# Kernel tuning notes

Hardware: AMD Instinct MI355X
Metric: run time of the kernel (lower is better)

Reference implementation:

```python
import jax, jax.numpy as jnp
import numpy as np

B, N, C = 4, 2047, 1024
H = 16
D = C // H  # head_dim = 64
SCALE = D ** -0.5


def setup_inputs() -> dict:
    key = jax.random.key(0)
    ks = jax.random.split(key, 5)
    return {
        "x": jax.random.normal(ks[0], (B, N, C), dtype=jnp.float32),
        "qkv_w": jax.random.normal(ks[1], (3 * C, C), dtype=jnp.float32) * (C ** -0.5),
        "proj_w": jax.random.normal(ks[2], (C, C), dtype=jnp.float32) * (C ** -0.5),
        "proj_b": jax.random.normal(ks[3], (C,), dtype=jnp.float32) * 0.02,
        "bias": jax.random.normal(ks[4], (H, N, N), dtype=jnp.float32) * 0.02,
    }


def reference(x, qkv_w, proj_w, proj_b, bias):
    b, n, c = x.shape
    qkv = (x @ qkv_w.T).reshape(b, n, 3, H, D)
    qkv = jnp.transpose(qkv, (2, 0, 3, 1, 4))
    q, k, v = qkv[0], qkv[1], qkv[2]
    q = q * SCALE
    # scores (B,H,N,N) + additive relative-position bias (H,N,N)
    attn = jnp.einsum('bhnd,bhmd->bhnm', q, k) + bias[None]
    attn = jax.nn.softmax(attn, axis=-1)
    out = jnp.einsum('bhnm,bhmd->bhnd', attn, v)
    out = jnp.transpose(out, (0, 2, 1, 3)).reshape(b, n, c)
    return out @ proj_w.T + proj_b
```

## Files before the change

### kernel.cpp

```cpp
#include <hip/hip_runtime.h>
#include <hip/hip_bf16.h>

typedef __bf16 bf16;
typedef __attribute__((ext_vector_type(8))) __bf16 bf16x8;
typedef __attribute__((ext_vector_type(4))) __bf16 bf16x4;
typedef __attribute__((ext_vector_type(4))) float f32x4;

#define MFMA16(a, b, c) __builtin_amdgcn_mfma_f32_16x16x32_bf16((a), (b), (c), 0, 0, 0)

constexpr int Bb = 4, Nn = 2047, Cc = 1024, Hh = 16, Dd = 64;
constexpr int M_ROWS = Bb * Nn;
constexpr int NPAD = 2048;
constexpr float SCALE = 0.125f;
constexpr float NEG_BIG = -1e30f;
constexpr float DEFER_THR = 8.0f;

template <bool V> struct BC { static constexpr bool value = V; };

__device__ inline bf16x8 bzero8() {
    bf16x8 v;
    for (int i = 0; i < 8; ++i) v[i] = (bf16)0.0f;
    return v;
}
__device__ inline bf16x8 bones8() {
    bf16x8 v;
    for (int i = 0; i < 8; ++i) v[i] = (bf16)1.0f;
    return v;
}
__device__ inline f32x4 fzero4() {
    f32x4 v = {0.f, 0.f, 0.f, 0.f};
    return v;
}

__device__ __forceinline__ void async_copy16(const void* g, void* l) {
    __builtin_amdgcn_global_load_lds(
        (const __attribute__((address_space(1))) unsigned int*)g,
        (__attribute__((address_space(3))) unsigned int*)l, 16, 0, 0);
}

__global__ __launch_bounds__(256) void cvt3_kernel(
    const float* __restrict__ a, bf16* __restrict__ oa, int na8,
    const float* __restrict__ b, bf16* __restrict__ ob, int nb8,
    const float* __restrict__ c, bf16* __restrict__ oc, int nc8) {
    int i = blockIdx.x * blockDim.x + threadIdx.x;
    const float* src;
    bf16* dst;
    int j = i;
    if (j < na8) {
        src = a; dst = oa;
    } else {
        j -= na8;
        if (j < nb8) {
            src = b; dst = ob;
        } else {
            j -= nb8;
            if (j >= nc8) return;
            src = c; dst = oc;
        }
    }
    float4 x0 = ((const float4*)src)[2 * (size_t)j];
    float4 x1 = ((const float4*)src)[2 * (size_t)j + 1];
    bf16x8 v;
    v[0] = (bf16)x0.x; v[1] = (bf16)x0.y; v[2] = (bf16)x0.z; v[3] = (bf16)x0.w;
    v[4] = (bf16)x1.x; v[5] = (bf16)x1.y; v[6] = (bf16)x1.z; v[7] = (bf16)x1.w;
    *(bf16x8*)(dst + 8 * (size_t)j) = v;
}

__global__ __launch_bounds__(256) void transpose_v_kernel(
    const bf16* __restrict__ vd, bf16* __restrict__ vtd) {
    __shared__ bf16 t[64 * 72];
    const int bh = blockIdx.x, nt = blockIdx.y;
    const int tid = threadIdx.x;
    const bf16* src = vd + (size_t)bh * Nn * Dd;
    bf16* dst = vtd + (size_t)bh * Dd * NPAD;
    int c = tid;
    for (int it = 0; it < 2; ++it, c += 256) {
        int row = c >> 3, d8 = (c & 7) * 8;
        int gn = nt * 64 + row;
        bf16x8 v = bzero8();
        if (gn < Nn) v = *(const bf16x8*)(src + (size_t)gn * Dd + d8);
        *(bf16x8*)(t + row * 72 + d8) = v;
    }
    __syncthreads();
    c = tid;
    for (int it = 0; it < 2; ++it, c += 256) {
        int d = c >> 3, j8 = (c & 7) * 8;
        bf16x8 v;
        for (int k = 0; k < 8; ++k) v[k] = t[(j8 + k) * 72 + d];
        *(bf16x8*)(dst + (size_t)d * NPAD + nt * 64 + j8) = v;
    }
}

template <int NOUT, int MODE>
__global__ __launch_bounds__(256, 2) void gemm_kernel(
    const bf16* __restrict__ A, const bf16* __restrict__ W,
    const float* __restrict__ pb, bf16* __restrict__ qd, bf16* __restrict__ kd,
    bf16* __restrict__ vd, float* __restrict__ outd) {
    constexpr int Kdim = 1024;
    __shared__ bf16 As[128 * 32];
    __shared__ bf16 Bs[128 * 32];

    const int tid = threadIdx.x;
    const int wave = tid >> 6, lane = tid & 63;
    const int quad = lane >> 4, l16 = lane & 15;
    const int m0 = blockIdx.y * 128;
    const int n0 = blockIdx.x * 128;
    const int wm = (wave >> 1) * 64, wn = (wave & 1) * 64;

    const int dma_r = lane >> 2;
    const int dma_k = (lane & 3) * 8;

    f32x4 acc[4][4];
    for (int mi = 0; mi < 4; ++mi)
        for (int ni = 0; ni < 4; ++ni) acc[mi][ni] = fzero4();

    for (int kb = 0; kb < Kdim; kb += 32) {
        __syncthreads();
        for (int i = 0; i < 2; ++i) {
            int g = wave * 2 + i;
            int row = g * 16 + dma_r;
            int gm = m0 + row;
            if (gm > M_ROWS - 1) gm = M_ROWS - 1;
            async_copy16(A + (size_t)gm * Kdim + kb + dma_k, As + g * 16 * 32);
        }
        for (int i = 0; i < 2; ++i) {
            int g = wave * 2 + i;
            int row = g * 16 + dma_r;
            async_copy16(W + (size_t)(n0 + row) * Kdim + kb + dma_k,
                         Bs + g * 16 * 32);
        }
        __syncthreads();

        bf16x8 af[4], bfr[4];
        for (int mi = 0; mi < 4; ++mi)
            af[mi] = *(const bf16x8*)(As + (wm + mi * 16 + l16) * 32 + quad * 8);
        for (int ni = 0; ni < 4; ++ni)
            bfr[ni] = *(const bf16x8*)(Bs + (wn + ni * 16 + l16) * 32 + quad * 8);
        for (int mi = 0; mi < 4; ++mi)
            for (int ni = 0; ni < 4; ++ni)
                acc[mi][ni] = MFMA16(af[mi], bfr[ni], acc[mi][ni]);
    }

    for (int mi = 0; mi < 4; ++mi) {
        for (int r = 0; r < 4; ++r) {
            int gm = m0 + wm + mi * 16 + quad * 4 + r;
            if (gm >= M_ROWS) continue;
            int bb = gm / Nn;
            int nn = gm - bb * Nn;
            for (int ni = 0; ni < 4; ++ni) {
                int gn = n0 + wn + ni * 16 + l16;
                float val = acc[mi][ni][r];
                if (MODE == 0) {
                    int which = gn >> 10;
                    int hh = (gn >> 6) & 15;
                    int dd = gn & 63;
                    size_t dst = ((size_t)(bb * Hh + hh) * Nn + nn) * Dd + dd;
                    if (which == 0)
                        qd[dst] = (bf16)(val * SCALE);
                    else if (which == 1)
                        kd[dst] = (bf16)val;
                    else
                        vd[dst] = (bf16)val;
                } else {
                    outd[(size_t)gm * NOUT + gn] = val + pb[gn];
                }
            }
        }
    }
}

__global__ __launch_bounds__(256, 4) void attn_kernel(
    const bf16* __restrict__ q, const bf16* __restrict__ kk,
    const bf16* __restrict__ vt, const float* __restrict__ bias,
    bf16* __restrict__ out) {
    __shared__ bf16 Ks[64 * 72];
    __shared__ bf16 VTs[64 * 72];
    __shared__ bf16 Ps[64 * 72];

    const int tid = threadIdx.x;
    const int wave = tid >> 6, lane = tid & 63;
    const int quad = lane >> 4, l16 = lane & 15;

    const int flat = blockIdx.x;
    const int xcd = flat & 7;
    const int sidx = flat >> 3;
    const int pair = xcd * 64 + (sidx >> 2);
    const int b = sidx & 3;
    const int qt = pair & 31;
    const int h = pair >> 5;

    const int q0 = qt * 64;
    const int wq0 = wave * 16;

    const size_t head_off = (size_t)(b * Hh + h) * Nn * Dd;
    const bf16* qh = q + head_off;
    const bf16* kh = kk + head_off;
    const bf16* vth = vt + (size_t)(b * Hh + h) * Dd * NPAD;

    int gq_lane = q0 + wq0 + l16;
    if (gq_lane > Nn - 1) gq_lane = Nn - 1;
    const float* brow = bias + ((size_t)h * Nn + gq_lane) * Nn;

    const int srow = tid >> 3;
    const int sd8 = (tid & 7) * 8;

    const bf16* qrow = qh + (size_t)gq_lane * Dd;
    const bf16x8 bq0 = *(const bf16x8*)(qrow + quad * 8);
    const bf16x8 bq1 = *(const bf16x8*)(qrow + 32 + quad * 8);
    const bf16x8 ones = bones8();

    bf16x8 pk0, pk1, pv0, pv1;
    float4 bp[4];

    auto issue_kv_fast = [&](int kvn) {
        int g0 = kvn + srow, g1 = g0 + 32;
        pk0 = *(const bf16x8*)(kh + (size_t)g0 * Dd + sd8);
        pk1 = *(const bf16x8*)(kh + (size_t)g1 * Dd + sd8);
        pv0 = *(const bf16x8*)(vth + (size_t)srow * NPAD + kvn + sd8);
        pv1 = *(const bf16x8*)(vth + (size_t)(srow + 32) * NPAD + kvn + sd8);
    };
    auto issue_kv_last = [&](int kvn) {
        int g0 = kvn + srow, g1 = g0 + 32;
        pk0 = bzero8();
        pk1 = bzero8();
        if (g0 < Nn) pk0 = *(const bf16x8*)(kh + (size_t)g0 * Dd + sd8);
        if (g1 < Nn) pk1 = *(const bf16x8*)(kh + (size_t)g1 * Dd + sd8);
        pv0 = *(const bf16x8*)(vth + (size_t)srow * NPAD + kvn + sd8);
        pv1 = *(const bf16x8*)(vth + (size_t)(srow + 32) * NPAD + kvn + sd8);
    };
    auto issue_bias = [&](int tn) {
        const int kvn = tn * 64;
        if (tn < 31) {
            for (int mi = 0; mi < 4; ++mi)
                bp[mi] = *(const float4*)(brow + kvn + mi * 16 + quad * 4);
        } else {
            for (int mi = 0; mi < 4; ++mi) {
                int base = kvn + mi * 16 + quad * 4;
                float4 f;
                f.x = (base + 0 < Nn) ? brow[base + 0] : 0.f;
                f.y = (base + 1 < Nn) ? brow[base + 1] : 0.f;
                f.z = (base + 2 < Nn) ? brow[base + 2] : 0.f;
                f.w = (base + 3 < Nn) ? brow[base + 3] : 0.f;
                bp[mi] = f;
            }
        }
    };

    issue_kv_fast(0);
    issue_bias(0);

    f32x4 acc_o[4];
    for (int nd = 0; nd < 4; ++nd) acc_o[nd] = fzero4();
    f32x4 acc_l = fzero4();
    float m_run = NEG_BIG;

    auto tile = [&](int t, auto lastc) {
        constexpr bool LAST = decltype(lastc)::value;
        const int kv0 = t * 64;
        __syncthreads();

        *(bf16x8*)(Ks + srow * 72 + sd8) = pk0;
        *(bf16x8*)(Ks + (srow + 32) * 72 + sd8) = pk1;
        *(bf16x8*)(VTs + srow * 72 + sd8) = pv0;
        *(bf16x8*)(VTs + (srow + 32) * 72 + sd8) = pv1;

        f32x4 cin[4];
        for (int mi = 0; mi < 4; ++mi) {
            cin[mi][0] = bp[mi].x; cin[mi][1] = bp[mi].y;
            cin[mi][2] = bp[mi].z; cin[mi][3] = bp[mi].w;
        }

        __syncthreads();

        if (!LAST) {
            if (t + 1 < 31) issue_kv_fast(kv0 + 64);
            else issue_kv_last(kv0 + 64);
            issue_bias(t + 1);
        }

        f32x4 sT[4];
        __builtin_amdgcn_s_setprio(1);
        for (int mi = 0; mi < 4; ++mi) {
            bf16x8 ak0 = *(const bf16x8*)(Ks + (mi * 16 + l16) * 72 + quad * 8);
            bf16x8 ak1 = *(const bf16x8*)(Ks + (mi * 16 + l16) * 72 + 32 + quad * 8);
            sT[mi] = MFMA16(ak0, bq0, cin[mi]);
            sT[mi] = MFMA16(ak1, bq1, sT[mi]);
        }
        __builtin_amdgcn_s_setprio(0);

        float s[4][4];
        for (int mi = 0; mi < 4; ++mi)
            for (int r = 0; r < 4; ++r) {
                if (LAST) {
                    int kv = kv0 + mi * 16 + quad * 4 + r;
                    s[mi][r] = (kv < Nn) ? sT[mi][r] : NEG_BIG;
                } else {
                    s[mi][r] = sT[mi][r];
                }
            }

        float mx = s[0][0];
        for (int mi = 0; mi < 4; ++mi)
            for (int r = 0; r < 4; ++r) mx = fmaxf(mx, s[mi][r]);
        mx = fmaxf(mx, __shfl_xor(mx, 16));
        mx = fmaxf(mx, __shfl_xor(mx, 32));
        float mnew = fmaxf(m_run, mx);

        float m_old = m_run;
        bool need = !__all(mnew - m_run <= DEFER_THR);
        if (need) m_run = mnew;

        for (int mi = 0; mi < 4; ++mi) {
            bf16x4 pv;
            for (int r = 0; r < 4; ++r)
                pv[r] = (bf16)__expf(s[mi][r] - m_run);
            *(bf16x4*)(Ps + (wq0 + l16) * 72 + mi * 16 + quad * 4) = pv;
        }

        if (need) {
            float alpha_col = __expf(m_old - m_run);
            float ar[4];
            for (int r = 0; r < 4; ++r) ar[r] = __shfl(alpha_col, quad * 4 + r);
            for (int nd = 0; nd < 4; ++nd)
                for (int r = 0; r < 4; ++r) acc_o[nd][r] *= ar[r];
            for (int r = 0; r < 4; ++r) acc_l[r] *= ar[r];
        }

        bf16x8 ap0 = *(const bf16x8*)(Ps + (wq0 + l16) * 72 + quad * 8);
        bf16x8 ap1 = *(const bf16x8*)(Ps + (wq0 + l16) * 72 + 32 + quad * 8);
        __builtin_amdgcn_s_setprio(1);
        for (int nd = 0; nd < 4; ++nd) {
            bf16x8 bv0 = *(const bf16x8*)(VTs + (nd * 16 + l16) * 72 + quad * 8);
            bf16x8 bv1 = *(const bf16x8*)(VTs + (nd * 16 + l16) * 72 + 32 + quad * 8);
            acc_o[nd] = MFMA16(ap0, bv0, acc_o[nd]);
            acc_o[nd] = MFMA16(ap1, bv1, acc_o[nd]);
        }
        acc_l = MFMA16(ap0, ones, acc_l);
        acc_l = MFMA16(ap1, ones, acc_l);
        __builtin_amdgcn_s_setprio(0);
    };

    for (int t = 0; t < 31; ++t) tile(t, BC<false>{});
    tile(31, BC<true>{});

    for (int nd = 0; nd < 4; ++nd) {
        for (int r = 0; r < 4; ++r) {
            int gq = q0 + wq0 + quad * 4 + r;
            if (gq >= Nn) continue;
            float val = acc_o[nd][r] / acc_l[r];
            out[((size_t)b * Nn + gq) * Cc + h * 64 + nd * 16 + l16] = (bf16)val;
        }
    }
}

extern "C" void kernel_launch(void* const* d_in, const int* in_sizes, int n_in,
                              void* d_out, int out_size, void* d_ws,
                              size_t ws_size, hipStream_t stream) {
    const float* x = (const float*)d_in[0];
    const float* qkv_w = (const float*)d_in[1];
    const float* proj_w = (const float*)d_in[2];
    const float* proj_b = (const float*)d_in[3];
    const float* bias = (const float*)d_in[4];
    float* out = (float*)d_out;

    const size_t per = (size_t)Bb * Hh * Nn * Dd;
    const size_t nx = (size_t)M_ROWS * Cc;
    const size_t nqw = (size_t)3 * Cc * Cc;
    const size_t npw = (size_t)Cc * Cc;

    bf16* qkvwb = (bf16*)d_ws;
    bf16* projwb = qkvwb + nqw;
    bf16* qd = projwb + npw;
    bf16* kd = qd + per;
    bf16* vd = kd + per;
    bf16* ao = vd + per;
    bf16* xb = ao + nx;
    bf16* vtd = ao + nx;

    {
        int na8 = (int)(nx / 8), nb8 = (int)(nqw / 8), nc8 = (int)(npw / 8);
        int tot = na8 + nb8 + nc8;
        cvt3_kernel<<<(tot + 255) / 256, 256, 0, stream>>>(
            x, xb, na8, qkv_w, qkvwb, nb8, proj_w, projwb, nc8);
    }
    gemm_kernel<3072, 0><<<dim3(24, 64), 256, 0, stream>>>(
        xb, qkvwb, nullptr, qd, kd, vd, nullptr);
    transpose_v_kernel<<<dim3(64, 32), 256, 0, stream>>>(vd, vtd);
    attn_kernel<<<dim3(2048), 256, 0, stream>>>(qd, kd, vtd, bias, ao);
    gemm_kernel<1024, 1><<<dim3(8, 64), 256, 0, stream>>>(
        ao, projwb, proj_b, nullptr, nullptr, nullptr, out);
}
```

Measured before the change: 634.2 us.

## Load K/V fragments straight into registers and drop LDS staging barriers

The attention kernel no longer stages K and V tiles through shared memory. Each wave now loads its own MFMA operand fragments for K and V directly from global memory, prefetching the next tile's K and bias after the QK MFMAs and the next V after the PV MFMAs, which removes both per-tile __syncthreads. The cost is fourfold redundant K/V global/L2 traffic across the waves of a block and higher register pressure, and the launch-bounds occupancy hint is loosened. The final tile also reads one K row past the end of each head without zero-fill, relying on the score mask to hide it.

```diff
diff --git a/kernel.cpp b/kernel.cpp
--- a/kernel.cpp
+++ b/kernel.cpp
@@ -169,12 +169,10 @@
     }
 }
 
-__global__ __launch_bounds__(256, 4) void attn_kernel(
+__global__ __launch_bounds__(256) void attn_kernel(
     const bf16* __restrict__ q, const bf16* __restrict__ kk,
     const bf16* __restrict__ vt, const float* __restrict__ bias,
     bf16* __restrict__ out) {
-    __shared__ bf16 Ks[64 * 72];
-    __shared__ bf16 VTs[64 * 72];
     __shared__ bf16 Ps[64 * 72];
 
     const int tid = threadIdx.x;
@@ -201,52 +199,53 @@
     if (gq_lane > Nn - 1) gq_lane = Nn - 1;
     const float* brow = bias + ((size_t)h * Nn + gq_lane) * Nn;
 
-    const int srow = tid >> 3;
-    const int sd8 = (tid & 7) * 8;
-
     const bf16* qrow = qh + (size_t)gq_lane * Dd;
     const bf16x8 bq0 = *(const bf16x8*)(qrow + quad * 8);
     const bf16x8 bq1 = *(const bf16x8*)(qrow + 32 + quad * 8);
     const bf16x8 ones = bones8();
 
-    bf16x8 pk0, pk1, pv0, pv1;
-    float4 bp[4];
-
-    auto issue_kv_fast = [&](int kvn) {
-        int g0 = kvn + srow, g1 = g0 + 32;
-        pk0 = *(const bf16x8*)(kh + (size_t)g0 * Dd + sd8);
-        pk1 = *(const bf16x8*)(kh + (size_t)g1 * Dd + sd8);
-        pv0 = *(const bf16x8*)(vth + (size_t)srow * NPAD + kvn + sd8);
-        pv1 = *(const bf16x8*)(vth + (size_t)(srow + 32) * NPAD + kvn + sd8);
+    bf16x8 ak[4][2];
+    bf16x8 av[4][2];
+    f32x4 bp[4];
+
+    auto issue_k = [&](int kvn) {
+#pragma unroll
+        for (int mi = 0; mi < 4; ++mi)
+#pragma unroll
+            for (int hf = 0; hf < 2; ++hf)
+                ak[mi][hf] = *(const bf16x8*)(
+                    kh + (size_t)(kvn + mi * 16 + l16) * Dd + hf * 32 + quad * 8);
     };
-    auto issue_kv_last = [&](int kvn) {
-        int g0 = kvn + srow, g1 = g0 + 32;
-        pk0 = bzero8();
-        pk1 = bzero8();
-        if (g0 < Nn) pk0 = *(const bf16x8*)(kh + (size_t)g0 * Dd + sd8);
-        if (g1 < Nn) pk1 = *(const bf16x8*)(kh + (size_t)g1 * Dd + sd8);
-        pv0 = *(const bf16x8*)(vth + (size_t)srow * NPAD + kvn + sd8);
-        pv1 = *(const bf16x8*)(vth + (size_t)(srow + 32) * NPAD + kvn + sd8);
+    auto issue_v = [&](int kvn) {
+#pragma unroll
+        for (int nd = 0; nd < 4; ++nd)
+#pragma unroll
+            for (int hf = 0; hf < 2; ++hf)
+                av[nd][hf] = *(const bf16x8*)(
+                    vth + (size_t)(nd * 16 + l16) * NPAD + kvn + hf * 32 + quad * 8);
     };
     auto issue_bias = [&](int tn) {
         const int kvn = tn * 64;
         if (tn < 31) {
+#pragma unroll
             for (int mi = 0; mi < 4; ++mi)
-                bp[mi] = *(const float4*)(brow + kvn + mi * 16 + quad * 4);
+                bp[mi] = *(const f32x4*)(brow + kvn + mi * 16 + quad * 4);
         } else {
+#pragma unroll
             for (int mi = 0; mi < 4; ++mi) {
                 int base = kvn + mi * 16 + quad * 4;
-                float4 f;
-                f.x = (base + 0 < Nn) ? brow[base + 0] : 0.f;
-                f.y = (base + 1 < Nn) ? brow[base + 1] : 0.f;
-                f.z = (base + 2 < Nn) ? brow[base + 2] : 0.f;
-                f.w = (base + 3 < Nn) ? brow[base + 3] : 0.f;
+                f32x4 f;
+                f[0] = (base + 0 < Nn) ? brow[base + 0] : 0.f;
+                f[1] = (base + 1 < Nn) ? brow[base + 1] : 0.f;
+                f[2] = (base + 2 < Nn) ? brow[base + 2] : 0.f;
+                f[3] = (base + 3 < Nn) ? brow[base + 3] : 0.f;
                 bp[mi] = f;
             }
         }
     };
 
-    issue_kv_fast(0);
+    issue_k(0);
+    issue_v(0);
     issue_bias(0);
 
     f32x4 acc_o[4];
@@ -257,51 +256,36 @@
     auto tile = [&](int t, auto lastc) {
         constexpr bool LAST = decltype(lastc)::value;
         const int kv0 = t * 64;
-        __syncthreads();
-
-        *(bf16x8*)(Ks + srow * 72 + sd8) = pk0;
-        *(bf16x8*)(Ks + (srow + 32) * 72 + sd8) = pk1;
-        *(bf16x8*)(VTs + srow * 72 + sd8) = pv0;
-        *(bf16x8*)(VTs + (srow + 32) * 72 + sd8) = pv1;
-
-        f32x4 cin[4];
-        for (int mi = 0; mi < 4; ++mi) {
-            cin[mi][0] = bp[mi].x; cin[mi][1] = bp[mi].y;
-            cin[mi][2] = bp[mi].z; cin[mi][3] = bp[mi].w;
-        }
-
-        __syncthreads();
-
-        if (!LAST) {
-            if (t + 1 < 31) issue_kv_fast(kv0 + 64);
-            else issue_kv_last(kv0 + 64);
-            issue_bias(t + 1);
-        }
 
         f32x4 sT[4];
         __builtin_amdgcn_s_setprio(1);
+#pragma unroll
         for (int mi = 0; mi < 4; ++mi) {
-            bf16x8 ak0 = *(const bf16x8*)(Ks + (mi * 16 + l16) * 72 + quad * 8);
-            bf16x8 ak1 = *(const bf16x8*)(Ks + (mi * 16 + l16) * 72 + 32 + quad * 8);
-            sT[mi] = MFMA16(ak0, bq0, cin[mi]);
-            sT[mi] = MFMA16(ak1, bq1, sT[mi]);
+            sT[mi] = MFMA16(ak[mi][0], bq0, bp[mi]);
+            sT[mi] = MFMA16(ak[mi][1], bq1, sT[mi]);
         }
         __builtin_amdgcn_s_setprio(0);
 
-        float s[4][4];
+        if (!LAST) {
+            issue_k(kv0 + 64);
+            issue_bias(t + 1);
+        }
+
+        if (LAST) {
+#pragma unroll
+            for (int mi = 0; mi < 4; ++mi)
+#pragma unroll
+                for (int r = 0; r < 4; ++r) {
+                    int kv = kv0 + mi * 16 + quad * 4 + r;
+                    if (kv >= Nn) sT[mi][r] = NEG_BIG;
+                }
+        }
+
+        float mx = sT[0][0];
+#pragma unroll
         for (int mi = 0; mi < 4; ++mi)
-            for (int r = 0; r < 4; ++r) {
-                if (LAST) {
-                    int kv = kv0 + mi * 16 + quad * 4 + r;
-                    s[mi][r] = (kv < Nn) ? sT[mi][r] : NEG_BIG;
-                } else {
-                    s[mi][r] = sT[mi][r];
-                }
-            }
-
-        float mx = s[0][0];
-        for (int mi = 0; mi < 4; ++mi)
-            for (int r = 0; r < 4; ++r) mx = fmaxf(mx, s[mi][r]);
+#pragma unroll
+            for (int r = 0; r < 4; ++r) mx = fmaxf(mx, sT[mi][r]);
         mx = fmaxf(mx, __shfl_xor(mx, 16));
         mx = fmaxf(mx, __shfl_xor(mx, 32));
         float mnew = fmaxf(m_run, mx);
@@ -310,34 +294,41 @@
         bool need = !__all(mnew - m_run <= DEFER_THR);
         if (need) m_run = mnew;
 
+#pragma unroll
         for (int mi = 0; mi < 4; ++mi) {
             bf16x4 pv;
+#pragma unroll
             for (int r = 0; r < 4; ++r)
-                pv[r] = (bf16)__expf(s[mi][r] - m_run);
+                pv[r] = (bf16)__expf(sT[mi][r] - m_run);
             *(bf16x4*)(Ps + (wq0 + l16) * 72 + mi * 16 + quad * 4) = pv;
         }
 
         if (need) {
             float alpha_col = __expf(m_old - m_run);
             float ar[4];
+#pragma unroll
             for (int r = 0; r < 4; ++r) ar[r] = __shfl(alpha_col, quad * 4 + r);
+#pragma unroll
             for (int nd = 0; nd < 4; ++nd)
+#pragma unroll
                 for (int r = 0; r < 4; ++r) acc_o[nd][r] *= ar[r];
+#pragma unroll
             for (int r = 0; r < 4; ++r) acc_l[r] *= ar[r];
         }
 
         bf16x8 ap0 = *(const bf16x8*)(Ps + (wq0 + l16) * 72 + quad * 8);
         bf16x8 ap1 = *(const bf16x8*)(Ps + (wq0 + l16) * 72 + 32 + quad * 8);
         __builtin_amdgcn_s_setprio(1);
+#pragma unroll
         for (int nd = 0; nd < 4; ++nd) {
-            bf16x8 bv0 = *(const bf16x8*)(VTs + (nd * 16 + l16) * 72 + quad * 8);
-            bf16x8 bv1 = *(const bf16x8*)(VTs + (nd * 16 + l16) * 72 + 32 + quad * 8);
-            acc_o[nd] = MFMA16(ap0, bv0, acc_o[nd]);
-            acc_o[nd] = MFMA16(ap1, bv1, acc_o[nd]);
+            acc_o[nd] = MFMA16(ap0, av[nd][0], acc_o[nd]);
+            acc_o[nd] = MFMA16(ap1, av[nd][1], acc_o[nd]);
         }
         acc_l = MFMA16(ap0, ones, acc_l);
         acc_l = MFMA16(ap1, ones, acc_l);
         __builtin_amdgcn_s_setprio(0);
+
+        if (!LAST) issue_v(kv0 + 64);
     };
 
     for (int t = 0; t < 31; ++t) tile(t, BC<false>{});
```

Result: slower. 978.5 us (+54.3%).

## Keep P in registers via lane shuffles and compute transposed O accumulator

Applied to the files above, without the earlier changes.

The softmax probability tile is no longer staged through shared memory. Each lane packs its bf16 probabilities into 64-bit words and exchanges them with cross-lane shuffles to form the MFMA B operand. The PV product is computed transposed (V^T times P), so each lane owns one query column. The rescale factor then needs no shuffle and the output is written as vector bf16x4 stores. This removes LDS writes and reads for P and frees LDS, in exchange for extra shuffle instructions and register pressure.

```diff
diff --git a/kernel.cpp b/kernel.cpp
--- a/kernel.cpp
+++ b/kernel.cpp
@@ -175,7 +175,6 @@
     bf16* __restrict__ out) {
     __shared__ bf16 Ks[64 * 72];
     __shared__ bf16 VTs[64 * 72];
-    __shared__ bf16 Ps[64 * 72];
 
     const int tid = threadIdx.x;
     const int wave = tid >> 6, lane = tid & 63;
@@ -231,9 +230,11 @@
     auto issue_bias = [&](int tn) {
         const int kvn = tn * 64;
         if (tn < 31) {
+#pragma unroll
             for (int mi = 0; mi < 4; ++mi)
                 bp[mi] = *(const float4*)(brow + kvn + mi * 16 + quad * 4);
         } else {
+#pragma unroll
             for (int mi = 0; mi < 4; ++mi) {
                 int base = kvn + mi * 16 + quad * 4;
                 float4 f;
@@ -249,10 +250,14 @@
     issue_kv_fast(0);
     issue_bias(0);
 
-    f32x4 acc_o[4];
-    for (int nd = 0; nd < 4; ++nd) acc_o[nd] = fzero4();
+    f32x4 acc_oT[4];
+    for (int nd = 0; nd < 4; ++nd) acc_oT[nd] = fzero4();
     f32x4 acc_l = fzero4();
     float m_run = NEG_BIG;
+
+    const int la = ((quad & 1) * 2) * 16 + l16;
+    const int lb = la + 16;
+    const bool hiSel = (quad >> 1) != 0;
 
     auto tile = [&](int t, auto lastc) {
         constexpr bool LAST = decltype(lastc)::value;
@@ -265,6 +270,7 @@
         *(bf16x8*)(VTs + (srow + 32) * 72 + sd8) = pv1;
 
         f32x4 cin[4];
+#pragma unroll
         for (int mi = 0; mi < 4; ++mi) {
             cin[mi][0] = bp[mi].x; cin[mi][1] = bp[mi].y;
             cin[mi][2] = bp[mi].z; cin[mi][3] = bp[mi].w;
@@ -280,6 +286,7 @@
 
         f32x4 sT[4];
         __builtin_amdgcn_s_setprio(1);
+#pragma unroll
         for (int mi = 0; mi < 4; ++mi) {
             bf16x8 ak0 = *(const bf16x8*)(Ks + (mi * 16 + l16) * 72 + quad * 8);
             bf16x8 ak1 = *(const bf16x8*)(Ks + (mi * 16 + l16) * 72 + 32 + quad * 8);
@@ -288,20 +295,21 @@
         }
         __builtin_amdgcn_s_setprio(0);
 
-        float s[4][4];
+        if (LAST) {
+#pragma unroll
+            for (int mi = 0; mi < 4; ++mi)
+#pragma unroll
+                for (int r = 0; r < 4; ++r) {
+                    int kv = kv0 + mi * 16 + quad * 4 + r;
+                    if (kv >= Nn) sT[mi][r] = NEG_BIG;
+                }
+        }
+
+        float mx = sT[0][0];
+#pragma unroll
         for (int mi = 0; mi < 4; ++mi)
-            for (int r = 0; r < 4; ++r) {
-                if (LAST) {
-                    int kv = kv0 + mi * 16 + quad * 4 + r;
-                    s[mi][r] = (kv < Nn) ? sT[mi][r] : NEG_BIG;
-                } else {
-                    s[mi][r] = sT[mi][r];
-                }
-            }
-
-        float mx = s[0][0];
-        for (int mi = 0; mi < 4; ++mi)
-            for (int r = 0; r < 4; ++r) mx = fmaxf(mx, s[mi][r]);
+#pragma unroll
+            for (int r = 0; r < 4; ++r) mx = fmaxf(mx, sT[mi][r]);
         mx = fmaxf(mx, __shfl_xor(mx, 16));
         mx = fmaxf(mx, __shfl_xor(mx, 32));
         float mnew = fmaxf(m_run, mx);
@@ -310,45 +318,65 @@
         bool need = !__all(mnew - m_run <= DEFER_THR);
         if (need) m_run = mnew;
 
+        unsigned long long pv64[4];
+#pragma unroll
         for (int mi = 0; mi < 4; ++mi) {
-            bf16x4 pv;
+            union { bf16x4 v; unsigned long long u; } pk;
+#pragma unroll
             for (int r = 0; r < 4; ++r)
-                pv[r] = (bf16)__expf(s[mi][r] - m_run);
-            *(bf16x4*)(Ps + (wq0 + l16) * 72 + mi * 16 + quad * 4) = pv;
+                pk.v[r] = (bf16)__expf(sT[mi][r] - m_run);
+            pv64[mi] = pk.u;
         }
 
         if (need) {
-            float alpha_col = __expf(m_old - m_run);
-            float ar[4];
-            for (int r = 0; r < 4; ++r) ar[r] = __shfl(alpha_col, quad * 4 + r);
+            float alpha = __expf(m_old - m_run);
+#pragma unroll
             for (int nd = 0; nd < 4; ++nd)
-                for (int r = 0; r < 4; ++r) acc_o[nd][r] *= ar[r];
-            for (int r = 0; r < 4; ++r) acc_l[r] *= ar[r];
-        }
-
-        bf16x8 ap0 = *(const bf16x8*)(Ps + (wq0 + l16) * 72 + quad * 8);
-        bf16x8 ap1 = *(const bf16x8*)(Ps + (wq0 + l16) * 72 + 32 + quad * 8);
+#pragma unroll
+                for (int r = 0; r < 4; ++r) acc_oT[nd][r] *= alpha;
+#pragma unroll
+            for (int r = 0; r < 4; ++r) acc_l[r] *= alpha;
+        }
+
+        bf16x8 B2[2];
+#pragma unroll
+        for (int hf = 0; hf < 2; ++hf) {
+            unsigned long long lo0 = __shfl(pv64[2 * hf + 0], la);
+            unsigned long long lo1 = __shfl(pv64[2 * hf + 1], la);
+            unsigned long long hi0 = __shfl(pv64[2 * hf + 0], lb);
+            unsigned long long hi1 = __shfl(pv64[2 * hf + 1], lb);
+            union { bf16x8 v; unsigned long long u[2]; } cat;
+            cat.u[0] = hiSel ? lo1 : lo0;
+            cat.u[1] = hiSel ? hi1 : hi0;
+            B2[hf] = cat.v;
+        }
+
         __builtin_amdgcn_s_setprio(1);
+#pragma unroll
         for (int nd = 0; nd < 4; ++nd) {
-            bf16x8 bv0 = *(const bf16x8*)(VTs + (nd * 16 + l16) * 72 + quad * 8);
-            bf16x8 bv1 = *(const bf16x8*)(VTs + (nd * 16 + l16) * 72 + 32 + quad * 8);
-            acc_o[nd] = MFMA16(ap0, bv0, acc_o[nd]);
-            acc_o[nd] = MFMA16(ap1, bv1, acc_o[nd]);
-        }
-        acc_l = MFMA16(ap0, ones, acc_l);
-        acc_l = MFMA16(ap1, ones, acc_l);
+            bf16x8 av0 = *(const bf16x8*)(VTs + (nd * 16 + l16) * 72 + quad * 8);
+            bf16x8 av1 = *(const bf16x8*)(VTs + (nd * 16 + l16) * 72 + 32 + quad * 8);
+            acc_oT[nd] = MFMA16(av0, B2[0], acc_oT[nd]);
+            acc_oT[nd] = MFMA16(av1, B2[1], acc_oT[nd]);
+        }
+        acc_l = MFMA16(ones, B2[0], acc_l);
+        acc_l = MFMA16(ones, B2[1], acc_l);
         __builtin_amdgcn_s_setprio(0);
     };
 
     for (int t = 0; t < 31; ++t) tile(t, BC<false>{});
     tile(31, BC<true>{});
 
-    for (int nd = 0; nd < 4; ++nd) {
-        for (int r = 0; r < 4; ++r) {
-            int gq = q0 + wq0 + quad * 4 + r;
-            if (gq >= Nn) continue;
-            float val = acc_o[nd][r] / acc_l[r];
-            out[((size_t)b * Nn + gq) * Cc + h * 64 + nd * 16 + l16] = (bf16)val;
+    if (q0 + wq0 + l16 < Nn) {
+        const float linv = 1.0f / acc_l[0];
+        bf16* orow = out + ((size_t)b * Nn + (q0 + wq0 + l16)) * Cc + h * 64;
+#pragma unroll
+        for (int nd = 0; nd < 4; ++nd) {
+            bf16x4 ov;
+#pragma unroll
+            for (int r = 0; r < 4; ++r)
+                ov[r] = (bf16)(acc_oT[nd][r] * linv);
+            *(bf16x4*)(orow + nd * 16 + quad * 4) = ov;
         }
     }
 }
```

Result: no change. 630.1 us (-0.6%).
